# Performance work log

Hardware: AMD Instinct MI355X
Metric: run time of the kernel (lower is better)

Reference implementation:

```python
import jax, jax.numpy as jnp
import numpy as np

C = 512        # channels
CTX = 768      # context_dim


def setup_inputs() -> dict:
    key = jax.random.key(0)
    ks = jax.random.split(key, 10)
    B, H, W = 8, 64, 64
    Lc = 512
    s = 0.02
    return {
        "x": jax.random.normal(ks[0], (B, C, H, W), jnp.float32),
        "context": jax.random.normal(ks[1], (B, Lc, CTX), jnp.float32),
        "Wq": jax.random.normal(ks[2], (C, C), jnp.float32) * s,
        "bq": jnp.zeros((C,), jnp.float32),
        "Wk": jax.random.normal(ks[3], (CTX, C), jnp.float32) * s,
        "bk": jnp.zeros((C,), jnp.float32),
        "Wv": jax.random.normal(ks[4], (CTX, C), jnp.float32) * s,
        "bv": jnp.zeros((C,), jnp.float32),
        "Wo": jax.random.normal(ks[5], (C, C), jnp.float32) * s,
        "bo": jnp.zeros((C,), jnp.float32),
    }


def reference(x, context, Wq, bq, Wk, bk, Wv, bv, Wo, bo):
    B, Cdim, H, W = x.shape
    scale = Cdim ** (-0.5)
    # [B, HW, C]
    xr = x.reshape(B, Cdim, H * W).transpose(0, 2, 1)
    q = xr @ Wq + bq                      # [B, HW, C]
    k = context @ Wk + bk                 # [B, Lc, C]
    v = context @ Wv + bv                 # [B, Lc, C]
    sim = jnp.einsum('bqc,bkc->bqk', q, k) * scale
    attn = jax.nn.softmax(sim, axis=-1)
    out = jnp.einsum('bqk,bkc->bqc', attn, v)
    out = out @ Wo + bo                   # [B, HW, C]
    out = out.transpose(0, 2, 1).reshape(B, Cdim, H, W)
    return x + out
```

## Files before the change

kernel.cpp:

```cpp
#include <hip/hip_runtime.h>
#include <hip/hip_bf16.h>

typedef __bf16 bf16_t;
typedef bf16_t bf16x8 __attribute__((ext_vector_type(8)));
typedef bf16_t bf16x4 __attribute__((ext_vector_type(4)));
typedef float  f32x4  __attribute__((ext_vector_type(4)));

constexpr int B_ = 8, C_ = 512, HW_ = 4096, LC_ = 512, CTX_ = 768;


__global__ void k_transpose_w(const float* __restrict__ in, bf16_t* __restrict__ out,
                              int R, int Cc) {
    __shared__ float t[32][33];
    int r0 = blockIdx.x * 32, c0 = blockIdx.y * 32;
    int tx = threadIdx.x, ty = threadIdx.y;
#pragma unroll
    for (int i = 0; i < 4; ++i)
        t[ty + i * 8][tx] = in[(size_t)(r0 + ty + i * 8) * Cc + c0 + tx];
    __syncthreads();
#pragma unroll
    for (int i = 0; i < 4; ++i)
        out[(size_t)(c0 + ty + i * 8) * R + r0 + tx] = (bf16_t)t[tx][ty + i * 8];
}

__global__ void k_bias(const float* __restrict__ bk, const float* __restrict__ bv,
                       const float* __restrict__ Wo, const float* __restrict__ bo,
                       float* __restrict__ bkvo) {
    int c = blockIdx.x * 256 + threadIdx.x;
    if (c >= 1024) return;
    if (c < 512) { bkvo[c] = bk[c]; return; }
    int cc = c - 512;
    float s = bo[cc];
    for (int m = 0; m < C_; ++m) s += bv[m] * Wo[(size_t)m * C_ + cc];
    bkvo[c] = s;
}

__global__ void k_f32_to_bf16(const float* __restrict__ in, bf16_t* __restrict__ out, int n) {
    int i = (blockIdx.x * 256 + threadIdx.x) * 4;
    if (i >= n) return;
    f32x4 v = *(const f32x4*)(in + i);
    bf16x4 w;
    w[0] = (bf16_t)v.x; w[1] = (bf16_t)v.y; w[2] = (bf16_t)v.z; w[3] = (bf16_t)v.w;
    *(bf16x4*)(out + i) = w;
}

__global__ void k_transpose_x(const float* __restrict__ x, bf16_t* __restrict__ xt) {
    __shared__ float t[32][33];
    int b = blockIdx.z;
    int p0 = blockIdx.x * 32, c0 = blockIdx.y * 32;
    const float* xb = x + (size_t)b * C_ * HW_;
    bf16_t* xtb = xt + (size_t)b * HW_ * C_;
    int tx = threadIdx.x, ty = threadIdx.y;
#pragma unroll
    for (int i = 0; i < 4; ++i) {
        int c = c0 + ty + i * 8;
        t[ty + i * 8][tx] = xb[(size_t)c * HW_ + p0 + tx];
    }
    __syncthreads();
#pragma unroll
    for (int i = 0; i < 4; ++i) {
        int p = p0 + ty + i * 8;
        xtb[(size_t)p * C_ + c0 + tx] = (bf16_t)t[tx][ty + i * 8];
    }
}

template <int MODE>
__global__ __launch_bounds__(256) void k_gemm(
    const bf16_t* __restrict__ A, int lda, long sA,
    const bf16_t* __restrict__ Bt, int ldb, long sB,
    const float* __restrict__ bias,
    void* __restrict__ out_, long sOut,
    int N, int K, float scale) {
    __shared__ bf16_t lA[128 * 32];
    __shared__ bf16_t lB[128 * 32];
    const int z = blockIdx.z;
    A  += (size_t)z * sA;
    Bt += (size_t)z * sB;
    const int tid  = threadIdx.x;
    const int lane = tid & 63;
    const int wave = tid >> 6;
    const int wm = (wave >> 1) * 64, wn = (wave & 1) * 64;
    const int bm0 = blockIdx.y * 128, bn0 = blockIdx.x * 128;
    const int ar = lane & 15, kc = lane >> 4;

    auto lA3 = (__attribute__((address_space(3))) char*)&lA[0];
    auto lB3 = (__attribute__((address_space(3))) char*)&lB[0];

    f32x4 acc[4][4] = {};

    for (int k0 = 0; k0 < K; k0 += 32) {
        __syncthreads();
#pragma unroll
        for (int s = 0; s < 2; ++s) {
            int wchunk = wave * 2 + s;
            int id = wchunk * 64 + lane;
            int row = id >> 2, c4 = id & 3;
            __builtin_amdgcn_global_load_lds(
                (const __attribute__((address_space(1))) void*)
                    &A[(size_t)(bm0 + row) * lda + k0 + c4 * 8],
                (__attribute__((address_space(3))) void*)(lA3 + wchunk * 1024),
                16, 0, 0);
            __builtin_amdgcn_global_load_lds(
                (const __attribute__((address_space(1))) void*)
                    &Bt[(size_t)(bn0 + row) * ldb + k0 + c4 * 8],
                (__attribute__((address_space(3))) void*)(lB3 + wchunk * 1024),
                16, 0, 0);
        }
        __syncthreads();
        bf16x8 af[4], bfr[4];
#pragma unroll
        for (int f = 0; f < 4; ++f) {
            af[f]  = *(const bf16x8*)&lA[(wm + f * 16 + ar) * 32 + kc * 8];
            bfr[f] = *(const bf16x8*)&lB[(wn + f * 16 + ar) * 32 + kc * 8];
        }
#pragma unroll
        for (int fm = 0; fm < 4; ++fm)
#pragma unroll
            for (int fn = 0; fn < 4; ++fn)
                acc[fm][fn] = __builtin_amdgcn_mfma_f32_16x16x32_bf16(
                    af[fm], bfr[fn], acc[fm][fn], 0, 0, 0);
    }

    const int rj = (lane >> 4) * 4;
    const int cj = lane & 15;

#pragma unroll
    for (int fm = 0; fm < 4; ++fm) {
#pragma unroll
        for (int fn = 0; fn < 4; ++fn) {
            int r0 = bm0 + wm + fm * 16 + rj;
            int cc = bn0 + wn + fn * 16 + cj;
            if constexpr (MODE == 3) {
                bf16_t* out = (bf16_t*)out_;
                bf16x4 v;
#pragma unroll
                for (int j = 0; j < 4; ++j) v[j] = (bf16_t)acc[fm][fn][j];
                *(bf16x4*)&out[(size_t)cc * sOut + r0] = v;
            } else {
                float bb = bias[cc];
                if (cc < 512) {
                    bf16_t* o = (bf16_t*)out_;
#pragma unroll
                    for (int j = 0; j < 4; ++j)
                        o[(size_t)(r0 + j) * 512 + cc] = (bf16_t)(acc[fm][fn][j] + bb);
                } else {
                    bf16_t* o = (bf16_t*)out_ + (size_t)B_ * LC_ * C_;
                    int b = r0 >> 9, l0 = r0 & 511;
                    bf16x4 v;
#pragma unroll
                    for (int j = 0; j < 4; ++j) v[j] = (bf16_t)(acc[fm][fn][j] + bb);
                    *(bf16x4*)&o[((size_t)b * C_ + (cc - 512)) * LC_ + l0] = v;
                }
            }
        }
    }
}

__global__ __launch_bounds__(512, 2) void k_flash(
    const bf16_t* __restrict__ xt, const bf16_t* __restrict__ Wq_t,
    const float* __restrict__ bq,
    const bf16_t* __restrict__ Kb, const bf16_t* __restrict__ Vt,
    const float* __restrict__ x, float* __restrict__ out) {
    __shared__ bf16_t lQP[64 * 512];
    __shared__ bf16_t lS[3][16384];
    float (*redA)[64] = (float(*)[64])&lQP[0];
    float (*redB)[64] = (float(*)[64])&lQP[512];

    const int bid = blockIdx.x;
    const int z = bid & 7;
    const int q0 = (bid >> 3) * 64;
    const int tid = threadIdx.x;
    const int lane = tid & 63;
    const int wave = tid >> 6;
    const int wm2 = wave >> 2;
    const int wn4 = wave & 3;
    const int h = lane >> 4;
    const int r15 = lane & 15;

    const bf16_t* Az = xt + ((size_t)z * HW_ + q0) * C_;
    const bf16_t* Kz = Kb + (size_t)z * LC_ * C_;
    const bf16_t* Vz = Vt + (size_t)z * C_ * LC_;

    auto lQ3 = (__attribute__((address_space(3))) char*)&lQP[0];
    auto lS3 = (__attribute__((address_space(3))) char*)&lS[0][0];

    auto STAGE = [&](int b, const bf16_t* __restrict__ src, int t) {
#pragma unroll
        for (int s = 0; s < 4; ++s) {
            int id = s * 512 + tid;
            int row = id >> 2, c4 = id & 3;
            int c4s = c4 ^ (row & 3);
            __builtin_amdgcn_global_load_lds(
                (const __attribute__((address_space(1))) void*)
                    &src[(size_t)row * 512 + t * 32 + c4s * 8],
                (__attribute__((address_space(3))) void*)
                    (lS3 + b * 32768 + s * 8192 + wave * 1024),
                16, 0, 0);
        }
    };

    f32x4 acc[2][8];

    auto STEP = [&](int t, int buf) {
        bf16x8 af[2], bfr[8];
        int c16 = t * 4 + h;
#pragma unroll
        for (int m = 0; m < 2; ++m) {
            int row = wm2 * 32 + m * 16 + r15;
            int sc = (c16 & 56) | ((c16 ^ row) & 7);
            af[m] = *(const bf16x8*)&lQP[row * 512 + sc * 8];
        }
        const bf16_t* lb = &lS[buf][0];
#pragma unroll
        for (int n = 0; n < 8; ++n) {
            int row = wn4 * 128 + n * 16 + r15;
            bfr[n] = *(const bf16x8*)&lb[row * 32 + (h ^ (row & 3)) * 8];
        }
        __builtin_amdgcn_s_setprio(1);
#pragma unroll
        for (int m = 0; m < 2; ++m)
#pragma unroll
            for (int n = 0; n < 8; ++n)
                acc[m][n] = __builtin_amdgcn_mfma_f32_16x16x32_bf16(
                    af[m], bfr[n], acc[m][n], 0, 0, 0);
        __builtin_amdgcn_s_setprio(0);
    };

    auto PHASE = [&](const bf16_t* __restrict__ src, int off) {
        for (int t = 0; t <= 13; ++t) {
            STAGE((t + 2 + off) % 3, src, t + 2);
            STEP(t, (t + off) % 3);
            asm volatile("s_waitcnt vmcnt(4)" ::: "memory");
            __builtin_amdgcn_sched_barrier(0);
            __builtin_amdgcn_s_barrier();
            __builtin_amdgcn_sched_barrier(0);
        }
        STEP(14, (14 + off) % 3);
        asm volatile("s_waitcnt vmcnt(0)" ::: "memory");
        __builtin_amdgcn_sched_barrier(0);
        __builtin_amdgcn_s_barrier();
        __builtin_amdgcn_sched_barrier(0);
        STEP(15, (15 + off) % 3);
    };

#pragma unroll
    for (int t = 0; t < 8; ++t) {
        int row = wave * 8 + t;
        int c16 = (lane & 56) | ((lane ^ row) & 7);
        __builtin_amdgcn_global_load_lds(
            (const __attribute__((address_space(1))) void*)&Az[(size_t)row * C_ + c16 * 8],
            (__attribute__((address_space(3))) void*)(lQ3 + row * 1024),
            16, 0, 0);
    }
    STAGE(0, Wq_t, 0); STAGE(1, Wq_t, 1);
    __syncthreads();

#pragma unroll
    for (int m = 0; m < 2; ++m)
#pragma unroll
        for (int n = 0; n < 8; ++n) acc[m][n] = (f32x4)0.f;
    PHASE(Wq_t, 0);

    __syncthreads();
    STAGE(1, Kz, 0); STAGE(2, Kz, 1);
    {
        float bqv[8];
#pragma unroll
        for (int n = 0; n < 8; ++n) bqv[n] = bq[wn4 * 128 + n * 16 + r15];
#pragma unroll
        for (int m = 0; m < 2; ++m)
#pragma unroll
            for (int j = 0; j < 4; ++j) {
                int row = wm2 * 32 + m * 16 + h * 4 + j;
#pragma unroll
                for (int n = 0; n < 8; ++n) {
                    int col = wn4 * 128 + n * 16 + r15;
                    int c16 = col >> 3;
                    int sc = (c16 & 56) | ((c16 ^ row) & 7);
                    lQP[row * 512 + sc * 8 + (col & 7)] = (bf16_t)(acc[m][n][j] + bqv[n]);
                }
            }
    }
    __syncthreads();

#pragma unroll
    for (int m = 0; m < 2; ++m)
#pragma unroll
        for (int n = 0; n < 8; ++n) acc[m][n] = (f32x4)0.f;
    PHASE(Kz, 1);

    __syncthreads();
    STAGE(2, Vz, 0); STAGE(0, Vz, 1);
    const float scale = 0.044194173824159216f;
    float M[2][4], inv[2][4];
#pragma unroll
    for (int m = 0; m < 2; ++m)
#pragma unroll
        for (int j = 0; j < 4; ++j) {
            float v = -1e30f;
#pragma unroll
            for (int n = 0; n < 8; ++n) v = fmaxf(v, acc[m][n][j]);
#pragma unroll
            for (int o = 1; o < 16; o <<= 1) v = fmaxf(v, __shfl_xor(v, o));
            if (r15 == 0) redA[wn4][wm2 * 32 + m * 16 + h * 4 + j] = v;
        }
    __syncthreads();
#pragma unroll
    for (int m = 0; m < 2; ++m)
#pragma unroll
        for (int j = 0; j < 4; ++j) {
            int row = wm2 * 32 + m * 16 + h * 4 + j;
            M[m][j] = fmaxf(fmaxf(redA[0][row], redA[1][row]),
                            fmaxf(redA[2][row], redA[3][row]));
        }
#pragma unroll
    for (int m = 0; m < 2; ++m)
#pragma unroll
        for (int j = 0; j < 4; ++j) {
            float s = 0.f;
#pragma unroll
            for (int n = 0; n < 8; ++n) {
                float e = __expf((acc[m][n][j] - M[m][j]) * scale);
                acc[m][n][j] = e;
                s += e;
            }
#pragma unroll
            for (int o = 1; o < 16; o <<= 1) s += __shfl_xor(s, o);
            if (r15 == 0) redB[wn4][wm2 * 32 + m * 16 + h * 4 + j] = s;
        }
    __syncthreads();
#pragma unroll
    for (int m = 0; m < 2; ++m)
#pragma unroll
        for (int j = 0; j < 4; ++j) {
            int row = wm2 * 32 + m * 16 + h * 4 + j;
            inv[m][j] = 1.f / (redB[0][row] + redB[1][row] +
                               redB[2][row] + redB[3][row]);
        }
    __syncthreads();
#pragma unroll
    for (int m = 0; m < 2; ++m)
#pragma unroll
        for (int j = 0; j < 4; ++j) {
            int row = wm2 * 32 + m * 16 + h * 4 + j;
#pragma unroll
            for (int n = 0; n < 8; ++n) {
                int col = wn4 * 128 + n * 16 + r15;
                int c16 = col >> 3;
                int sc = (c16 & 56) | ((c16 ^ row) & 7);
                lQP[row * 512 + sc * 8 + (col & 7)] = (bf16_t)(acc[m][n][j] * inv[m][j]);
            }
        }
    __syncthreads();

#pragma unroll
    for (int m = 0; m < 2; ++m)
#pragma unroll
        for (int n = 0; n < 8; ++n) acc[m][n] = (f32x4)0.f;
    PHASE(Vz, 2);

    float* oz = out + (size_t)z * C_ * HW_;
    const float* xz = x + (size_t)z * C_ * HW_;
#pragma unroll
    for (int m = 0; m < 2; ++m)
#pragma unroll
        for (int n = 0; n < 8; ++n) {
            int r0 = q0 + wm2 * 32 + m * 16 + h * 4;
            int cc = wn4 * 128 + n * 16 + r15;
            f32x4 xv = *(const f32x4*)&xz[(size_t)cc * HW_ + r0];
            f32x4 o;
#pragma unroll
            for (int j = 0; j < 4; ++j) o[j] = acc[m][n][j] + xv[j];
            *(f32x4*)&oz[(size_t)cc * HW_ + r0] = o;
        }
}

extern "C" void kernel_launch(void* const* d_in, const int* in_sizes, int n_in,
                              void* d_out, int out_size, void* d_ws, size_t ws_size,
                              hipStream_t stream) {
    (void)in_sizes; (void)n_in; (void)out_size; (void)ws_size;
    const float* x   = (const float*)d_in[0];
    const float* ctx = (const float*)d_in[1];
    const float* Wq  = (const float*)d_in[2];
    const float* bq  = (const float*)d_in[3];
    const float* Wk  = (const float*)d_in[4];
    const float* bk  = (const float*)d_in[5];
    const float* Wv  = (const float*)d_in[6];
    const float* bv  = (const float*)d_in[7];
    const float* Wo  = (const float*)d_in[8];
    const float* bo  = (const float*)d_in[9];
    float* out = (float*)d_out;

    char* ws = (char*)d_ws;
    size_t off = 0;
    auto alloc = [&](size_t bytes) {
        char* p = ws + off;
        off += (bytes + 255) & ~(size_t)255;
        return p;
    };
    bf16_t* Wq_t  = (bf16_t*)alloc((size_t)C_ * C_ * 2);
    bf16_t* Wk_t  = (bf16_t*)alloc((size_t)C_ * CTX_ * 2);
    bf16_t* Wvo_t = (bf16_t*)alloc((size_t)C_ * CTX_ * 2);
    bf16_t* Wv_b  = (bf16_t*)alloc((size_t)CTX_ * C_ * 2);
    bf16_t* Wo_t  = (bf16_t*)alloc((size_t)C_ * C_ * 2);
    float*  bkvo  = (float*)alloc((size_t)1024 * 4);
    bf16_t* ctxb  = (bf16_t*)alloc((size_t)B_ * LC_ * CTX_ * 2);
    bf16_t* xt    = (bf16_t*)alloc((size_t)B_ * HW_ * C_ * 2);
    bf16_t* Kb    = (bf16_t*)alloc((size_t)B_ * LC_ * C_ * 2);
    bf16_t* Vt    = (bf16_t*)alloc((size_t)B_ * C_ * LC_ * 2);

    k_transpose_w<<<dim3(C_ / 32, C_ / 32), dim3(32, 8), 0, stream>>>(Wq, Wq_t, C_, C_);
    k_transpose_w<<<dim3(CTX_ / 32, C_ / 32), dim3(32, 8), 0, stream>>>(Wk, Wk_t, CTX_, C_);
    k_transpose_w<<<dim3(C_ / 32, C_ / 32), dim3(32, 8), 0, stream>>>(Wo, Wo_t, C_, C_);
    k_f32_to_bf16<<<(CTX_ * C_ / 4 + 255) / 256, 256, 0, stream>>>(Wv, Wv_b, CTX_ * C_);
    k_bias<<<4, 256, 0, stream>>>(bk, bv, Wo, bo, bkvo);
    k_f32_to_bf16<<<(B_ * LC_ * CTX_ / 4 + 255) / 256, 256, 0, stream>>>(
        ctx, ctxb, B_ * LC_ * CTX_);
    k_transpose_x<<<dim3(HW_ / 32, C_ / 32, B_), dim3(32, 8), 0, stream>>>(x, xt);

    k_gemm<3><<<dim3(4, 6, 1), 256, 0, stream>>>(
        Wv_b, C_, 0, Wo_t, C_, 0, nullptr, Wvo_t, CTX_, C_, C_, 1.f);
    k_gemm<4><<<dim3(8, 32, 1), 256, 0, stream>>>(
        ctxb, CTX_, 0, Wk_t, CTX_, 0, bkvo, Kb, 0, 1024, CTX_, 1.f);
    k_flash<<<512, 512, 0, stream>>>(xt, Wq_t, bq, Kb, Vt, x, out);
}
```

Baseline: 196.5 us.

## Fuse x transpose into flash kernel, double-buffer LDS fragment reads, parallelize bias

Removes the separate x-transpose kernel and its bf16 intermediate buffer. The flash kernel now reads x directly in fp32, converts it and writes it into the swizzled LDS Q tile. The GEMM phase loop is restructured so the LDS fragment reads for the next step overlap the current MFMA batch, using two register fragment sets. The bias-folding kernel is rewritten to use many blocks with wave reductions over the transposed bf16 Wo, replacing a serial 512-iteration loop per thread. The trade-off is higher register pressure from the doubled fragments and strided fp32 global reads of x inside the main kernel.

```diff
diff --git a/kernel.cpp b/kernel.cpp
--- a/kernel.cpp
+++ b/kernel.cpp
@@ -24,15 +24,23 @@
 }
 
 __global__ void k_bias(const float* __restrict__ bk, const float* __restrict__ bv,
-                       const float* __restrict__ Wo, const float* __restrict__ bo,
+                       const bf16_t* __restrict__ Wo_t, const float* __restrict__ bo,
                        float* __restrict__ bkvo) {
-    int c = blockIdx.x * 256 + threadIdx.x;
-    if (c >= 1024) return;
-    if (c < 512) { bkvo[c] = bk[c]; return; }
-    int cc = c - 512;
-    float s = bo[cc];
-    for (int m = 0; m < C_; ++m) s += bv[m] * Wo[(size_t)m * C_ + cc];
-    bkvo[c] = s;
+    int blk = blockIdx.x, tid = threadIdx.x;
+    if (blk >= 128) {
+        int i = (blk - 128) * 256 + tid;
+        bkvo[i] = bk[i];
+        return;
+    }
+    int wave = tid >> 6, lane = tid & 63;
+    int cc = blk * 4 + wave;
+    bf16x8 w = *(const bf16x8*)&Wo_t[(size_t)cc * C_ + lane * 8];
+    float s = 0.f;
+#pragma unroll
+    for (int j = 0; j < 8; ++j) s += bv[lane * 8 + j] * (float)w[j];
+#pragma unroll
+    for (int o = 32; o > 0; o >>= 1) s += __shfl_xor(s, o);
+    if (lane == 0) bkvo[512 + cc] = s + bo[cc];
 }
 
 __global__ void k_f32_to_bf16(const float* __restrict__ in, bf16_t* __restrict__ out, int n) {
@@ -42,26 +50,6 @@
     bf16x4 w;
     w[0] = (bf16_t)v.x; w[1] = (bf16_t)v.y; w[2] = (bf16_t)v.z; w[3] = (bf16_t)v.w;
     *(bf16x4*)(out + i) = w;
-}
-
-__global__ void k_transpose_x(const float* __restrict__ x, bf16_t* __restrict__ xt) {
-    __shared__ float t[32][33];
-    int b = blockIdx.z;
-    int p0 = blockIdx.x * 32, c0 = blockIdx.y * 32;
-    const float* xb = x + (size_t)b * C_ * HW_;
-    bf16_t* xtb = xt + (size_t)b * HW_ * C_;
-    int tx = threadIdx.x, ty = threadIdx.y;
-#pragma unroll
-    for (int i = 0; i < 4; ++i) {
-        int c = c0 + ty + i * 8;
-        t[ty + i * 8][tx] = xb[(size_t)c * HW_ + p0 + tx];
-    }
-    __syncthreads();
-#pragma unroll
-    for (int i = 0; i < 4; ++i) {
-        int p = p0 + ty + i * 8;
-        xtb[(size_t)p * C_ + c0 + tx] = (bf16_t)t[tx][ty + i * 8];
-    }
 }
 
 template <int MODE>
@@ -157,8 +145,7 @@
 }
 
 __global__ __launch_bounds__(512, 2) void k_flash(
-    const bf16_t* __restrict__ xt, const bf16_t* __restrict__ Wq_t,
-    const float* __restrict__ bq,
+    const bf16_t* __restrict__ Wq_t, const float* __restrict__ bq,
     const bf16_t* __restrict__ Kb, const bf16_t* __restrict__ Vt,
     const float* __restrict__ x, float* __restrict__ out) {
     __shared__ bf16_t lQP[64 * 512];
@@ -177,11 +164,10 @@
     const int h = lane >> 4;
     const int r15 = lane & 15;
 
-    const bf16_t* Az = xt + ((size_t)z * HW_ + q0) * C_;
     const bf16_t* Kz = Kb + (size_t)z * LC_ * C_;
     const bf16_t* Vz = Vt + (size_t)z * C_ * LC_;
-
-    auto lQ3 = (__attribute__((address_space(3))) char*)&lQP[0];
+    const float*  xz = x + (size_t)z * C_ * HW_;
+
     auto lS3 = (__attribute__((address_space(3))) char*)&lS[0][0];
 
     auto STAGE = [&](int b, const bf16_t* __restrict__ src, int t) {
@@ -200,9 +186,9 @@
     };
 
     f32x4 acc[2][8];
-
-    auto STEP = [&](int t, int buf) {
-        bf16x8 af[2], bfr[8];
+    bf16x8 af0[2], bf0[8], af1[2], bf1[8];
+
+    auto READF = [&](bf16x8 (&af)[2], bf16x8 (&bfr)[8], int t, int buf) {
         int c16 = t * 4 + h;
 #pragma unroll
         for (int m = 0; m < 2; ++m) {
@@ -216,6 +202,8 @@
             int row = wn4 * 128 + n * 16 + r15;
             bfr[n] = *(const bf16x8*)&lb[row * 32 + (h ^ (row & 3)) * 8];
         }
+    };
+    auto MF = [&](bf16x8 (&af)[2], bf16x8 (&bfr)[8]) {
         __builtin_amdgcn_s_setprio(1);
 #pragma unroll
         for (int m = 0; m < 2; ++m)
@@ -225,34 +213,49 @@
                     af[m], bfr[n], acc[m][n], 0, 0, 0);
         __builtin_amdgcn_s_setprio(0);
     };
-
-    auto PHASE = [&](const bf16_t* __restrict__ src, int off) {
-        for (int t = 0; t <= 13; ++t) {
-            STAGE((t + 2 + off) % 3, src, t + 2);
-            STEP(t, (t + off) % 3);
-            asm volatile("s_waitcnt vmcnt(4)" ::: "memory");
-            __builtin_amdgcn_sched_barrier(0);
-            __builtin_amdgcn_s_barrier();
-            __builtin_amdgcn_sched_barrier(0);
-        }
-        STEP(14, (14 + off) % 3);
-        asm volatile("s_waitcnt vmcnt(0)" ::: "memory");
+    auto BAR = [&]() {
         __builtin_amdgcn_sched_barrier(0);
         __builtin_amdgcn_s_barrier();
         __builtin_amdgcn_sched_barrier(0);
-        STEP(15, (15 + off) % 3);
-    };
-
-#pragma unroll
-    for (int t = 0; t < 8; ++t) {
-        int row = wave * 8 + t;
-        int c16 = (lane & 56) | ((lane ^ row) & 7);
-        __builtin_amdgcn_global_load_lds(
-            (const __attribute__((address_space(1))) void*)&Az[(size_t)row * C_ + c16 * 8],
-            (__attribute__((address_space(3))) void*)(lQ3 + row * 1024),
-            16, 0, 0);
+    };
+
+    auto PHASE = [&](const bf16_t* __restrict__ src, int off) {
+        READF(af0, bf0, 0, off % 3);
+#pragma unroll
+        for (int tt = 0; tt < 7; ++tt) {
+            int t = 2 * tt;
+            STAGE((t + 2 + off) % 3, src, t + 2);
+            MF(af0, bf0);
+            asm volatile("s_waitcnt vmcnt(4)" ::: "memory");
+            READF(af1, bf1, t + 1, (t + 1 + off) % 3);
+            BAR();
+            STAGE((t + 3 + off) % 3, src, t + 3);
+            MF(af1, bf1);
+            asm volatile("s_waitcnt vmcnt(4)" ::: "memory");
+            READF(af0, bf0, t + 2, (t + 2 + off) % 3);
+            BAR();
+        }
+        MF(af0, bf0);
+        asm volatile("s_waitcnt vmcnt(0)" ::: "memory");
+        READF(af1, bf1, 15, (15 + off) % 3);
+        BAR();
+        MF(af1, bf1);
+    };
+
+    STAGE(0, Wq_t, 0); STAGE(1, Wq_t, 1);
+#pragma unroll
+    for (int i = 0; i < 16; ++i) {
+        int c = i * 32 + (tid >> 4);
+        int q = (tid & 15) * 4;
+        f32x4 v = *(const f32x4*)&xz[(size_t)c * HW_ + q0 + q];
+#pragma unroll
+        for (int j = 0; j < 4; ++j) {
+            int row = q + j;
+            int c16 = c >> 3;
+            int sc = (c16 & 56) | ((c16 ^ row) & 7);
+            lQP[row * 512 + sc * 8 + (c & 7)] = (bf16_t)v[j];
+        }
     }
-    STAGE(0, Wq_t, 0); STAGE(1, Wq_t, 1);
     __syncthreads();
 
 #pragma unroll
@@ -360,7 +363,6 @@
     PHASE(Vz, 2);
 
     float* oz = out + (size_t)z * C_ * HW_;
-    const float* xz = x + (size_t)z * C_ * HW_;
 #pragma unroll
     for (int m = 0; m < 2; ++m)
 #pragma unroll
@@ -405,7 +407,6 @@
     bf16_t* Wo_t  = (bf16_t*)alloc((size_t)C_ * C_ * 2);
     float*  bkvo  = (float*)alloc((size_t)1024 * 4);
     bf16_t* ctxb  = (bf16_t*)alloc((size_t)B_ * LC_ * CTX_ * 2);
-    bf16_t* xt    = (bf16_t*)alloc((size_t)B_ * HW_ * C_ * 2);
     bf16_t* Kb    = (bf16_t*)alloc((size_t)B_ * LC_ * C_ * 2);
     bf16_t* Vt    = (bf16_t*)alloc((size_t)B_ * C_ * LC_ * 2);
 
@@ -413,14 +414,13 @@
     k_transpose_w<<<dim3(CTX_ / 32, C_ / 32), dim3(32, 8), 0, stream>>>(Wk, Wk_t, CTX_, C_);
     k_transpose_w<<<dim3(C_ / 32, C_ / 32), dim3(32, 8), 0, stream>>>(Wo, Wo_t, C_, C_);
     k_f32_to_bf16<<<(CTX_ * C_ / 4 + 255) / 256, 256, 0, stream>>>(Wv, Wv_b, CTX_ * C_);
-    k_bias<<<4, 256, 0, stream>>>(bk, bv, Wo, bo, bkvo);
+    k_bias<<<130, 256, 0, stream>>>(bk, bv, Wo_t, bo, bkvo);
     k_f32_to_bf16<<<(B_ * LC_ * CTX_ / 4 + 255) / 256, 256, 0, stream>>>(
         ctx, ctxb, B_ * LC_ * CTX_);
-    k_transpose_x<<<dim3(HW_ / 32, C_ / 32, B_), dim3(32, 8), 0, stream>>>(x, xt);
 
     k_gemm<3><<<dim3(4, 6, 1), 256, 0, stream>>>(
         Wv_b, C_, 0, Wo_t, C_, 0, nullptr, Wvo_t, CTX_, C_, C_, 1.f);
     k_gemm<4><<<dim3(8, 32, 1), 256, 0, stream>>>(
         ctxb, CTX_, 0, Wk_t, CTX_, 0, bkvo, Kb, 0, 1024, CTX_, 1.f);
-    k_flash<<<512, 512, 0, stream>>>(xt, Wq_t, bq, Kb, Vt, x, out);
-}
+    k_flash<<<512, 512, 0, stream>>>(Wq_t, bq, Kb, Vt, x, out);
+}
```

Measured after the change: 165.6 us. -15.7%, faster.
